# Performance work log

Measured on AMD Instinct MI355X. Metric: run time of the kernel, lower is better.

## Reference

```python
import jax, jax.numpy as jnp
import numpy as np

NUM_ENTITIES = 100000
NUM_TIMES = 10000
D = 512
DB = 768
NUM_REL = 200
NUM_BASES = 4
N_NODES = 30000
N_EDGES = 200000
B = 128
P_ENT = 64
P_TIME = 32
T_UNIQ = 2000


def setup_inputs() -> dict:
    key = jax.random.key(0)
    ks = jax.random.split(key, 32)
    n = jax.random.normal
    ri = jax.random.randint
    inp = {}
    # learned params
    inp['emb'] = n(ks[0], (NUM_ENTITIES + NUM_TIMES, D), jnp.float32) * 0.05
    sc = 1.0 / np.sqrt(D)
    inp['basis1'] = n(ks[1], (NUM_BASES, D, D), jnp.float32) * sc
    inp['att1'] = n(ks[2], (NUM_REL, NUM_BASES), jnp.float32) * 0.5
    inp['root1'] = n(ks[3], (D, D), jnp.float32) * sc
    inp['bias1'] = jnp.zeros((D,), jnp.float32)
    inp['basis2'] = n(ks[4], (NUM_BASES, D, D), jnp.float32) * sc
    inp['att2'] = n(ks[5], (NUM_REL, NUM_BASES), jnp.float32) * 0.5
    inp['root2'] = n(ks[6], (D, D), jnp.float32) * sc
    inp['bias2'] = jnp.zeros((D,), jnp.float32)
    sb = 1.0 / np.sqrt(DB)
    inp['W_lin'] = n(ks[7], (DB, D), jnp.float32) * sb
    inp['b_lin'] = jnp.zeros((D,), jnp.float32)
    inp['W_attn'] = n(ks[8], (DB, D), jnp.float32) * sb
    inp['b_attn'] = jnp.zeros((D,), jnp.float32)
    inp['W_prob'] = n(ks[9], (DB, 1), jnp.float32) * sb
    inp['b_prob'] = jnp.zeros((1,), jnp.float32)
    # forward tensor args
    inp['ques_emb_bert'] = n(ks[10], (B, DB), jnp.float32)
    inp['x_idx'] = ri(ks[11], (N_NODES,), 0, NUM_ENTITIES, jnp.int32)
    inp['edge_index'] = ri(ks[12], (2, N_EDGES), 0, N_NODES, jnp.int32)
    inp['edge_type'] = ri(ks[13], (N_EDGES,), 0, NUM_REL, jnp.int32)
    inp['start_time'] = ri(ks[14], (N_EDGES,), 0, NUM_TIMES, jnp.int32)
    inp['end_time'] = ri(ks[15], (N_EDGES,), 0, NUM_TIMES, jnp.int32)
    inp['edge_batch_idx'] = jnp.sort(ri(ks[16], (N_EDGES,), 0, B, jnp.int32))
    inp['edge_norm'] = jax.random.uniform(ks[17], (N_EDGES,), jnp.float32)
    inp['uniq_times'] = ri(ks[18], (T_UNIQ,), 0, NUM_TIMES, jnp.int32)
    # padded index vectors: positions >= count point at the appended zero row
    ent_counts = ri(ks[19], (B,), 1, P_ENT + 1, jnp.int32)
    time_counts = ri(ks[20], (B,), 1, P_TIME + 1, jnp.int32)
    pe = ri(ks[21], (B, P_ENT), 0, N_NODES, jnp.int32)
    pt = ri(ks[22], (B, P_TIME), 0, T_UNIQ, jnp.int32)
    inp['padded_ent'] = jnp.where(jnp.arange(P_ENT)[None, :] < ent_counts[:, None], pe, N_NODES)
    inp['padded_time'] = jnp.where(jnp.arange(P_TIME)[None, :] < time_counts[:, None], pt, T_UNIQ)
    inp['ent_counts'] = ent_counts
    inp['time_counts'] = time_counts
    return inp


def rgcn_layer(x, basis, att, root, bias, src, dst, etype, st_emb, et_emb, q_t, edge_norm):
    # basis decomposition: project all nodes through each basis once. [N, NB, D]
    xb = jnp.einsum('ni,bio->nbo', x, basis)
    coeff = att[etype]                                 # [E, NB]
    msg = jnp.einsum('eb,ebd->ed', coeff, xb[src])     # [E, D]
    # time gate: question-time embedding vs edge interval midpoint embedding
    gate = jax.nn.sigmoid(jnp.sum(q_t * 0.5 * (st_emb + et_emb), axis=-1))  # [E]
    msg = msg * (gate * edge_norm)[:, None]
    agg = jax.ops.segment_sum(msg, dst, num_segments=N_NODES)
    return agg + x @ root + bias


def reference(emb, basis1, att1, root1, bias1, basis2, att2, root2, bias2,
              W_lin, b_lin, W_attn, b_attn, W_prob, b_prob,
              ques_emb_bert, x_idx, edge_index, edge_type, start_time, end_time,
              edge_batch_idx, edge_norm, uniq_times, padded_ent, padded_time,
              ent_counts, time_counts):
    question_embedding = ques_emb_bert @ W_lin + b_lin                  # [B, D]
    time_for_edge_attn = (ques_emb_bert @ W_attn + b_attn)[edge_batch_idx]  # [E, D]
    st_emb = emb[start_time + NUM_ENTITIES]
    et_emb = emb[end_time + NUM_ENTITIES]
    x = emb[x_idx]                                                      # [N, D]
    src, dst = edge_index[0], edge_index[1]
    h = jax.nn.relu(rgcn_layer(x, basis1, att1, root1, bias1, src, dst, edge_type,
                               st_emb, et_emb, time_for_edge_attn, edge_norm))
    # dropout is identity in eval mode
    h = rgcn_layer(h, basis2, att2, root2, bias2, src, dst, edge_type,
                   st_emb, et_emb, time_for_edge_attn, edge_norm)       # [N, D]
    subgraph_time_emb = emb[uniq_times + NUM_ENTITIES]                  # [T_u, D]
    zero = jnp.zeros((1, D), h.dtype)
    ent_w_zeros = jnp.concatenate([h, zero], axis=0)
    time_w_zeros = jnp.concatenate([subgraph_time_emb, zero], axis=0)
    pooled_ent = jnp.sum(ent_w_zeros[padded_ent], axis=1) / ent_counts[:, None].astype(h.dtype)
    pooled_time = jnp.sum(time_w_zeros[padded_time], axis=1) / time_counts[:, None].astype(h.dtype)
    p_ent = jax.nn.sigmoid(ques_emb_bert @ W_prob + b_prob)             # [B, 1]
    pred = (question_embedding + pooled_ent * p_ent + pooled_time * (1.0 - p_ent)) / 3.0
    # batched cosine similarity against full entity+time vocab
    pred_n = pred / jnp.maximum(jnp.linalg.norm(pred, axis=-1, keepdims=True), 1e-8)
    emb_n = emb / jnp.maximum(jnp.linalg.norm(emb, axis=-1, keepdims=True), 1e-8)
    score = pred_n @ emb_n.T                                            # [B, V]
    return score * 30.0
```

## Files before the change

### kernel.cpp

```cpp
#include <hip/hip_runtime.h>

#define NUM_ENT   100000
#define NTIMES    10000
#define DD        512
#define DB        768
#define NREL      200
#define NBAS      4
#define NN        30000
#define NEDGE     200000
#define BATCH     128
#define PENT      64
#define PTIME     32
#define TUNIQ     2000
#define V_TOT     110000
#define V_PAD     110208
#define VT16      6888
#define M_PAD     30080
#define KT_L      80
#define KT_E      16

typedef __attribute__((ext_vector_type(8))) short s8v;
typedef __attribute__((ext_vector_type(4))) float f4v;

__device__ __forceinline__ unsigned short f2bf(float x){
  unsigned int u = __builtin_bit_cast(unsigned int, x);
  u += 0x7fffu + ((u >> 16) & 1u);
  return (unsigned short)(u >> 16);
}
__device__ __forceinline__ float bf2f(unsigned short h){
  unsigned int u = ((unsigned int)h) << 16;
  return __builtin_bit_cast(float, u);
}

__device__ __forceinline__ void gload16(const void* g, void* l){
  __builtin_amdgcn_global_load_lds(
      (const __attribute__((address_space(1))) void*)g,
      (__attribute__((address_space(3))) void*)l, 16, 0, 0);
}


__global__ __launch_bounds__(256) void k_conv_emb(const float* __restrict__ emb,
    unsigned short* __restrict__ Bp, float* __restrict__ invn){
  int vt = blockIdx.x;
  int wid = threadIdx.x >> 6, lane = threadIdx.x & 63;
  int vrow = vt * 16 + (lane & 15);
  float ss = 0.f;
  __shared__ float ssw[4][16];
  for (int i = 0; i < 4; ++i){
    int kt = wid + i * 4;
    int k0 = kt * 32 + (lane >> 4) * 8;
    s8v o;
    if (vrow < V_TOT){
      const float* p = emb + (size_t)vrow * DD + k0;
      #pragma unroll
      for (int j = 0; j < 8; ++j){ float x = p[j]; ss += x * x; o[j] = (short)f2bf(x); }
    } else {
      #pragma unroll
      for (int j = 0; j < 8; ++j) o[j] = 0;
    }
    *reinterpret_cast<s8v*>(Bp + ((size_t)(kt * VT16 + vt) << 9) + lane * 8) = o;
  }
  ss += __shfl_xor(ss, 16);
  ss += __shfl_xor(ss, 32);
  if ((lane >> 4) == 0) ssw[wid][lane] = ss;
  __syncthreads();
  if (threadIdx.x < 16){
    float s = ssw[0][threadIdx.x] + ssw[1][threadIdx.x] + ssw[2][threadIdx.x] + ssw[3][threadIdx.x];
    int v = vt * 16 + threadIdx.x;
    invn[v] = (v < V_TOT) ? (1.0f / fmaxf(sqrtf(s), 1e-8f)) : 0.0f;
  }
}

__global__ __launch_bounds__(256) void k_small2(const float* __restrict__ ques,
    const float* __restrict__ Wl, const float* __restrict__ bl,
    const float* __restrict__ Wa, const float* __restrict__ ba,
    const float* __restrict__ Wp, const float* __restrict__ bp,
    float* __restrict__ qlin, float* __restrict__ qattn, float* __restrict__ pent){
  if (blockIdx.x == 32){
    int b = threadIdx.x >> 1, half = threadIdx.x & 1;
    float a = 0.f;
    int k0 = half * 384;
    for (int k = k0; k < k0 + 384; ++k)
      a = fmaf(ques[(size_t)b * DB + k], Wp[k], a);
    a += __shfl_xor(a, 1);
    if (half == 0) pent[b] = 1.f / (1.f + expf(-(a + bp[0])));
    return;
  }
  __shared__ float sq[128 * 96];
  int col = threadIdx.x & 31, bg = threadIdx.x >> 5;
  int c0 = blockIdx.x * 32;
  const float* W = (c0 < 512) ? Wl : Wa;
  int wcol = (c0 & 511) + col;
  float acc[16] = {};
  for (int k0 = 0; k0 < DB; k0 += 96){
    __syncthreads();
    for (int i = threadIdx.x; i < 128 * 96; i += 256){
      int b = i / 96, kk = i - b * 96;
      sq[i] = ques[(size_t)b * DB + k0 + kk];
    }
    __syncthreads();
    for (int kk = 0; kk < 96; kk += 4){
      float w0 = W[(size_t)(k0 + kk + 0) * 512 + wcol];
      float w1 = W[(size_t)(k0 + kk + 1) * 512 + wcol];
      float w2 = W[(size_t)(k0 + kk + 2) * 512 + wcol];
      float w3 = W[(size_t)(k0 + kk + 3) * 512 + wcol];
      #pragma unroll
      for (int bb = 0; bb < 16; ++bb){
        float4 qv = *reinterpret_cast<const float4*>(&sq[(bg * 16 + bb) * 96 + kk]);
        acc[bb] = fmaf(qv.x, w0, fmaf(qv.y, w1, fmaf(qv.z, w2, fmaf(qv.w, w3, acc[bb]))));
      }
    }
  }
  float* dst = (c0 < 512) ? qlin : qattn;
  const float* bias = (c0 < 512) ? bl : ba;
  #pragma unroll
  for (int bb = 0; bb < 16; ++bb)
    dst[(size_t)(bg * 16 + bb) * 512 + wcol] = acc[bb] + bias[wcol];
}

__global__ __launch_bounds__(256) void k_pack_qrows(const float* __restrict__ src,
    unsigned short* __restrict__ Ap){
  int w = (int)((blockIdx.x * 256 + threadIdx.x) >> 6);
  int lane = threadIdx.x & 63;
  if (w >= BATCH) return;
  const float* p = src + (size_t)w * 512 + lane * 8;
  s8v o;
  #pragma unroll
  for (int j = 0; j < 8; ++j) o[j] = (short)f2bf(p[j]);
  *reinterpret_cast<s8v*>(Ap + ((size_t)((w >> 4) * KT_E + (lane >> 2)) << 9)
                             + ((w & 15) + (lane & 3) * 16) * 8) = o;
}

__global__ __launch_bounds__(256) void k_pack_B(const float* __restrict__ basis,
    const float* __restrict__ root, unsigned short* __restrict__ Bp){
  int idx = blockIdx.x * 256 + threadIdx.x;
  if (idx >= KT_L * 32 * 64) return;
  int lane = idx & 63; int kt = idx >> 11;
  int k0 = kt * 32 + (lane >> 4) * 8;
  int col = ((idx >> 6) & 31) * 16 + (lane & 15);
  s8v o;
  #pragma unroll
  for (int j = 0; j < 8; ++j){
    int k = k0 + j;
    float v = (k < 2048) ? basis[(size_t)k * 512 + col] : root[(size_t)(k - 2048) * 512 + col];
    o[j] = (short)f2bf(v);
  }
  *reinterpret_cast<s8v*>(Bp + (size_t)idx * 8) = o;
}

template<int MODE, int SWZ>
__global__ __launch_bounds__(256) void k_gemm(
    const unsigned short* __restrict__ A, const unsigned short* __restrict__ B,
    int Kt, int Bt_stride, int ct_off,
    const float* __restrict__ bias, const float* __restrict__ invn,
    float* __restrict__ outf, unsigned short* __restrict__ outh){
  __shared__ __align__(1024) short sAll[3 * 8192];
  int tid = threadIdx.x;
  int lane = tid & 63, wid = tid >> 6;
  int wr = wid >> 1, wc = wid & 1;
  int rt0, ct0;
  if constexpr (SWZ){
    const int q = 117, r = 4;
    int g = blockIdx.x;
    int xcd = g & 7, i = g >> 3;
    int ng = (xcd < r ? xcd * (q + 1) : r * (q + 1) + (xcd - r) * q) + i;
    rt0 = (ng >> 2) * 8;
    ct0 = (ng & 3) * 8;
  } else {
    rt0 = blockIdx.x * 8;
    ct0 = blockIdx.y * 8;
  }
  int ctB = ct0 + ct_off;
  const unsigned short* pA0 = A + ((size_t)(rt0 + 2 * wid) * Kt) * 512 + lane * 8;
  const unsigned short* pA1 = pA0 + (size_t)Kt * 512;
  const unsigned short* pB0 = B + (size_t)(ctB + 2 * wid) * 512 + lane * 8;
  const unsigned short* pB1 = pB0 + 512;
  size_t gbs = (size_t)Bt_stride * 512;
  int so = 2 * wid * 512;
  f4v acc[4][4] = {};

  auto STAGE = [&](int buf, int kt){
    short* b = &sAll[buf * 8192];
    gload16(pA0 + (size_t)kt * 512, b + so);
    gload16(pA1 + (size_t)kt * 512, b + so + 512);
    gload16(pB0 + (size_t)kt * gbs, b + 4096 + so);
    gload16(pB1 + (size_t)kt * gbs, b + 4096 + so + 512);
  };
  auto COMPUTE = [&](int buf){
    const short* base = &sAll[buf * 8192];
    s8v af[4], bfr[4];
    #pragma unroll
    for (int m = 0; m < 4; ++m) af[m] = *reinterpret_cast<const s8v*>(base + (wr * 4 + m) * 512 + lane * 8);
    #pragma unroll
    for (int n = 0; n < 4; ++n) bfr[n] = *reinterpret_cast<const s8v*>(base + 4096 + (wc * 4 + n) * 512 + lane * 8);
    #pragma unroll
    for (int m = 0; m < 4; ++m)
      #pragma unroll
      for (int n = 0; n < 4; ++n)
        acc[m][n] = __builtin_amdgcn_mfma_f32_16x16x32_bf16(af[m], bfr[n], acc[m][n], 0, 0, 0);
  };

  STAGE(0, 0);
  STAGE(1, 1);
  int cb = 0, sb = 2;
  for (int kt = 0; kt < Kt - 2; ++kt){
    STAGE(sb, kt + 2);
    asm volatile("s_waitcnt vmcnt(8)" ::: "memory");
    __builtin_amdgcn_s_barrier();
    __builtin_amdgcn_sched_barrier(0);
    COMPUTE(cb);
    __builtin_amdgcn_s_barrier();
    cb = (cb == 2) ? 0 : cb + 1;
    sb = (sb == 2) ? 0 : sb + 1;
  }
  asm volatile("s_waitcnt vmcnt(4)" ::: "memory");
  __builtin_amdgcn_s_barrier();
  __builtin_amdgcn_sched_barrier(0);
  COMPUTE(cb);
  cb = (cb == 2) ? 0 : cb + 1;
  asm volatile("s_waitcnt vmcnt(0)" ::: "memory");
  __builtin_amdgcn_s_barrier();
  __builtin_amdgcn_sched_barrier(0);
  COMPUTE(cb);

  #pragma unroll
  for (int m = 0; m < 4; ++m)
    #pragma unroll
    for (int n = 0; n < 4; ++n){
      int row0 = rt0 * 16 + (wr * 4 + m) * 16 + ((lane >> 4) * 4);
      int col  = (ct0 + wc * 4 + n) * 16 + (lane & 15);
      #pragma unroll
      for (int r = 0; r < 4; ++r){
        float c = acc[m][n][r];
        int rr = row0 + r;
        if constexpr (MODE == 0){
          if (col < NTIMES) outf[(size_t)rr * NTIMES + col] = c;
        } else if constexpr (MODE == 1){
          if (rr < NN){ float v = fmaxf(c + bias[col], 0.f); outh[(size_t)rr * 512 + col] = f2bf(v); }
        } else if constexpr (MODE == 2){
          if (rr < NN) outf[(size_t)rr * 512 + col] = c + bias[col];
        } else {
          if (col < V_TOT) outf[(size_t)rr * V_TOT + col] = c * invn[col] * 30.0f;
        }
      }
    }
}

__global__ __launch_bounds__(256) void k_edge_w(const int* __restrict__ ebatch,
    const int* __restrict__ st, const int* __restrict__ et,
    const float* __restrict__ enorm, const float* __restrict__ M2,
    float* __restrict__ we){
  int e = blockIdx.x * 256 + threadIdx.x;
  if (e >= NEDGE) return;
  int b = ebatch[e];
  float s = 0.5f * (M2[(size_t)b * NTIMES + st[e]] + M2[(size_t)b * NTIMES + et[e]]);
  we[e] = (1.f / (1.f + expf(-s))) * enorm[e];
}

__global__ __launch_bounds__(256) void k_count(const int* __restrict__ ei,
    int* __restrict__ cnt, int* __restrict__ lists){
  int e = blockIdx.x * 256 + threadIdx.x;
  if (e >= NEDGE) return;
  int dst = ei[NEDGE + e];
  int slot = atomicAdd(&cnt[dst], 1);
  if (slot < 64) lists[(size_t)dst * 64 + slot] = e;
}

__global__ __launch_bounds__(256) void k_gather_x(const int* __restrict__ x_idx,
    const unsigned short* __restrict__ Bp, unsigned short* __restrict__ Ap,
    unsigned short* __restrict__ x_rm){
  int w = (int)((blockIdx.x * 256 + threadIdx.x) >> 6);
  int lane = threadIdx.x & 63;
  if (w >= NN) return;
  int v = x_idx[w];
  s8v x = *reinterpret_cast<const s8v*>(
      Bp + ((size_t)(lane >> 2) * VT16 + (v >> 4)) * 512 + ((v & 15) + (lane & 3) * 16) * 8);
  *reinterpret_cast<s8v*>(x_rm + (size_t)w * 512 + lane * 8) = x;
  *reinterpret_cast<s8v*>(Ap + ((size_t)(w >> 4) * KT_L + 64 + (lane >> 2)) * 512
                             + ((w & 15) + (lane & 3) * 16) * 8) = x;
}

__global__ __launch_bounds__(256) void k_pack_rows(const unsigned short* __restrict__ src_rm,
    unsigned short* __restrict__ Ap){
  int w = (int)((blockIdx.x * 256 + threadIdx.x) >> 6);
  int lane = threadIdx.x & 63;
  if (w >= NN) return;
  s8v x = *reinterpret_cast<const s8v*>(src_rm + (size_t)w * 512 + lane * 8);
  *reinterpret_cast<s8v*>(Ap + ((size_t)(w >> 4) * KT_L + 64 + (lane >> 2)) * 512
                             + ((w & 15) + (lane & 3) * 16) * 8) = x;
}

__global__ __launch_bounds__(256) void k_edge_agg(const unsigned short* __restrict__ xsrc,
    const int* __restrict__ ei, const int* __restrict__ etype,
    const float* __restrict__ we, const float* __restrict__ att,
    const int* __restrict__ cnt, const int* __restrict__ lists,
    unsigned short* __restrict__ Ap){
  __shared__ float satt[NREL * NBAS];
  __shared__ int sed[4][64];
  for (int i = threadIdx.x; i < NREL * NBAS; i += 256) satt[i] = att[i];
  int wid = threadIdx.x >> 6, lane = threadIdx.x & 63;
  int n = blockIdx.x * 4 + wid;
  int deg = min(cnt[n], 64);
  int eid = (lane < deg) ? lists[(size_t)n * 64 + lane] : 0x7fffffff;
  int rank = 0;
  for (int j = 0; j < 64; ++j){
    int v = __shfl(eid, j);
    rank += (v < eid) ? 1 : 0;
  }
  __syncthreads();
  if (lane < deg) sed[wid][rank] = eid;
  __syncthreads();
  float acc[NBAS][8] = {};
  if (deg > 0){
    int my_e = sed[wid][(lane < deg) ? lane : 0];
    int my_s = ei[my_e];
    int my_t = etype[my_e];
    float my_w = we[my_e];
    float c0l = my_w * satt[my_t * 4 + 0];
    float c1l = my_w * satt[my_t * 4 + 1];
    float c2l = my_w * satt[my_t * 4 + 2];
    float c3l = my_w * satt[my_t * 4 + 3];
    int s0 = __shfl(my_s, 0);
    s8v xv = *reinterpret_cast<const s8v*>(xsrc + (size_t)s0 * 512 + lane * 8);
    for (int j = 0; j < deg; ++j){
      s8v xn = xv;
      if (j + 1 < deg){
        int sn = __shfl(my_s, j + 1);
        xn = *reinterpret_cast<const s8v*>(xsrc + (size_t)sn * 512 + lane * 8);
      }
      float c0 = __shfl(c0l, j), c1 = __shfl(c1l, j);
      float c2 = __shfl(c2l, j), c3 = __shfl(c3l, j);
      #pragma unroll
      for (int jj = 0; jj < 8; ++jj){
        float x = bf2f((unsigned short)xv[jj]);
        acc[0][jj] = fmaf(c0, x, acc[0][jj]);
        acc[1][jj] = fmaf(c1, x, acc[1][jj]);
        acc[2][jj] = fmaf(c2, x, acc[2][jj]);
        acc[3][jj] = fmaf(c3, x, acc[3][jj]);
      }
      xv = xn;
    }
  }
  #pragma unroll
  for (int b = 0; b < NBAS; ++b){
    s8v o;
    #pragma unroll
    for (int jj = 0; jj < 8; ++jj) o[jj] = (short)f2bf(acc[b][jj]);
    *reinterpret_cast<s8v*>(Ap + ((size_t)(n >> 4) * KT_L + b * 16 + (lane >> 2)) * 512
                               + ((n & 15) + (lane & 3) * 16) * 8) = o;
  }
}

__global__ __launch_bounds__(256) void k_pred(const float* __restrict__ h2,
    const float* __restrict__ emb, const int* __restrict__ uniq,
    const int* __restrict__ pent_idx, const int* __restrict__ ptime_idx,
    const int* __restrict__ ent_c, const int* __restrict__ time_c,
    const float* __restrict__ qlin, const float* __restrict__ pent,
    unsigned short* __restrict__ Ap_pred){
  int w = (int)((blockIdx.x * 256 + threadIdx.x) >> 6);
  int lane = threadIdx.x & 63;
  if (w >= BATCH) return;
  float ae[8] = {}, at[8] = {};
  for (int j = 0; j < PENT; ++j){
    int idx = pent_idx[w * PENT + j];
    if (idx < NN){
      const float* p = h2 + (size_t)idx * 512 + lane * 8;
      #pragma unroll
      for (int jj = 0; jj < 8; ++jj) ae[jj] += p[jj];
    }
  }
  for (int j = 0; j < PTIME; ++j){
    int ti = ptime_idx[w * PTIME + j];
    if (ti < TUNIQ){
      const float* p = emb + (size_t)(NUM_ENT + uniq[ti]) * 512 + lane * 8;
      #pragma unroll
      for (int jj = 0; jj < 8; ++jj) at[jj] += p[jj];
    }
  }
  float ce = 1.f / (float)ent_c[w], ct = 1.f / (float)time_c[w];
  float p = pent[w];
  float pr[8]; float ss = 0.f;
  #pragma unroll
  for (int jj = 0; jj < 8; ++jj){
    float v = (qlin[(size_t)w * 512 + lane * 8 + jj] + ae[jj] * ce * p + at[jj] * ct * (1.f - p)) * (1.f / 3.f);
    pr[jj] = v; ss += v * v;
  }
  ss += __shfl_xor(ss, 32); ss += __shfl_xor(ss, 16); ss += __shfl_xor(ss, 8);
  ss += __shfl_xor(ss, 4);  ss += __shfl_xor(ss, 2);  ss += __shfl_xor(ss, 1);
  float inv = 1.f / fmaxf(sqrtf(ss), 1e-8f);
  s8v o;
  #pragma unroll
  for (int jj = 0; jj < 8; ++jj) o[jj] = (short)f2bf(pr[jj] * inv);
  *reinterpret_cast<s8v*>(Ap_pred + ((size_t)((w >> 4) * KT_E + (lane >> 2)) << 9)
                                  + ((w & 15) + (lane & 3) * 16) * 8) = o;
}

extern "C" void kernel_launch(void* const* d_in, const int* in_sizes, int n_in,
                              void* d_out, int out_size, void* d_ws, size_t ws_size,
                              hipStream_t stream){
  const float* emb    = (const float*)d_in[0];
  const float* basis1 = (const float*)d_in[1];
  const float* att1   = (const float*)d_in[2];
  const float* root1  = (const float*)d_in[3];
  const float* bias1  = (const float*)d_in[4];
  const float* basis2 = (const float*)d_in[5];
  const float* att2   = (const float*)d_in[6];
  const float* root2  = (const float*)d_in[7];
  const float* bias2  = (const float*)d_in[8];
  const float* W_lin  = (const float*)d_in[9];
  const float* b_lin  = (const float*)d_in[10];
  const float* W_attn = (const float*)d_in[11];
  const float* b_attn = (const float*)d_in[12];
  const float* W_prob = (const float*)d_in[13];
  const float* b_prob = (const float*)d_in[14];
  const float* ques   = (const float*)d_in[15];
  const int* x_idx    = (const int*)d_in[16];
  const int* eidx     = (const int*)d_in[17];
  const int* etype    = (const int*)d_in[18];
  const int* stime    = (const int*)d_in[19];
  const int* etime    = (const int*)d_in[20];
  const int* ebatch   = (const int*)d_in[21];
  const float* enorm  = (const float*)d_in[22];
  const int* uniq     = (const int*)d_in[23];
  const int* pent_i   = (const int*)d_in[24];
  const int* ptime_i  = (const int*)d_in[25];
  const int* ent_c    = (const int*)d_in[26];
  const int* time_c   = (const int*)d_in[27];
  float* out = (float*)d_out;

  char* w = (char*)d_ws;
  size_t off = 0;
  auto alloc = [&](size_t bytes)->char*{ char* p = w + off; off += (bytes + 255) & ~(size_t)255; return p; };
  unsigned short* Bp_emb = (unsigned short*)alloc((size_t)KT_E * VT16 * 1024);
  float*          invn   = (float*)alloc((size_t)V_PAD * 4);
  unsigned short* Ap     = (unsigned short*)alloc((size_t)(M_PAD / 16) * KT_L * 1024);
  unsigned short* B1p    = (unsigned short*)alloc((size_t)KT_L * 32 * 1024);
  unsigned short* B2p    = (unsigned short*)alloc((size_t)KT_L * 32 * 1024);
  char* xh_base = alloc((size_t)NN * 512 * 2 * 2);
  unsigned short* x_rm = (unsigned short*)xh_base;
  unsigned short* h1   = (unsigned short*)(xh_base + (size_t)NN * 512 * 2);
  float*          h2   = (float*)xh_base;
  float* M2    = (float*)alloc((size_t)BATCH * NTIMES * 4);
  float* we    = (float*)alloc((size_t)NEDGE * 4);
  float* qlin  = (float*)alloc((size_t)BATCH * 512 * 4);
  float* qattn = (float*)alloc((size_t)BATCH * 512 * 4);
  float* pent  = (float*)alloc(1024);
  unsigned short* Apq    = (unsigned short*)alloc((size_t)8 * KT_E * 1024);
  unsigned short* Appred = (unsigned short*)alloc((size_t)8 * KT_E * 1024);
  int* cnt   = (int*)alloc((size_t)NN * 4);
  int* lists = (int*)alloc((size_t)NN * 64 * 4);
  (void)ws_size; (void)in_sizes; (void)n_in; (void)out_size;

  k_conv_emb<<<VT16, 256, 0, stream>>>(emb, Bp_emb, invn);
  k_small2<<<33, 256, 0, stream>>>(ques, W_lin, b_lin, W_attn, b_attn, W_prob, b_prob,
                                   qlin, qattn, pent);
  k_pack_qrows<<<32, 256, 0, stream>>>(qattn, Apq);
  k_pack_B<<<(KT_L * 32 * 64 + 255) / 256, 256, 0, stream>>>(basis1, root1, B1p);
  k_pack_B<<<(KT_L * 32 * 64 + 255) / 256, 256, 0, stream>>>(basis2, root2, B2p);
  k_gemm<0,0><<<dim3(1, 79), 256, 0, stream>>>(Apq, Bp_emb, KT_E, VT16, NUM_ENT / 16,
                                               nullptr, nullptr, M2, nullptr);
  k_edge_w<<<(NEDGE + 255) / 256, 256, 0, stream>>>(ebatch, stime, etime, enorm, M2, we);
  hipMemsetAsync(cnt, 0, (size_t)NN * 4, stream);
  k_count<<<(NEDGE + 255) / 256, 256, 0, stream>>>(eidx, cnt, lists);
  k_gather_x<<<NN / 4, 256, 0, stream>>>(x_idx, Bp_emb, Ap, x_rm);
  k_edge_agg<<<NN / 4, 256, 0, stream>>>(x_rm, eidx, etype, we, att1, cnt, lists, Ap);
  k_gemm<1,1><<<940, 256, 0, stream>>>(Ap, B1p, KT_L, 32, 0,
                                       bias1, nullptr, nullptr, h1);
  k_pack_rows<<<NN / 4, 256, 0, stream>>>(h1, Ap);
  k_edge_agg<<<NN / 4, 256, 0, stream>>>(h1, eidx, etype, we, att2, cnt, lists, Ap);
  k_gemm<2,1><<<940, 256, 0, stream>>>(Ap, B2p, KT_L, 32, 0,
                                       bias2, nullptr, h2, nullptr);
  k_pred<<<32, 256, 0, stream>>>(h2, emb, uniq, pent_i, ptime_i, ent_c, time_c,
                                 qlin, pent, Appred);
  k_gemm<3,0><<<dim3(1, V_PAD / 128), 256, 0, stream>>>(Appred, Bp_emb, KT_E, VT16, 0,
                                                        nullptr, invn, out, nullptr);
}
```

Measured before the change: 789.0 us.

## Use 256x256-tile 512-thread GEMM for RGCN layers and store layer-2 output as bf16

The two RGCN layer GEMMs move from 128x128 tiles with 256 threads to 256x256 tiles with 512 threads (8 waves, 8x4 MFMA accumulators each). The grid is XCD-swizzled over 236 blocks, and s_setprio is raised around the MFMA loop. The aim is more data reuse per LDS load and less global traffic. The layer-2 output is now written as bf16 instead of fp32, which halves that write and the later reads in k_pred at some precision cost. Embedding conversion also switches to float4 loads. The A buffer grows to cover the padded rows of the larger tiles. The larger tiles bring more register pressure and only 236 blocks, which may underfill the CUs.

```diff
diff --git a/kernel.cpp b/kernel.cpp
--- a/kernel.cpp
+++ b/kernel.cpp
@@ -15,7 +15,8 @@
 #define V_TOT     110000
 #define V_PAD     110208
 #define VT16      6888
-#define M_PAD     30080
+#define M_PAD2    30208
+#define MT2R      1888
 #define KT_L      80
 #define KT_E      16
 
@@ -51,9 +52,14 @@
     int k0 = kt * 32 + (lane >> 4) * 8;
     s8v o;
     if (vrow < V_TOT){
-      const float* p = emb + (size_t)vrow * DD + k0;
-      #pragma unroll
-      for (int j = 0; j < 8; ++j){ float x = p[j]; ss += x * x; o[j] = (short)f2bf(x); }
+      const float4* p = reinterpret_cast<const float4*>(emb + (size_t)vrow * DD + k0);
+      float4 v0 = p[0], v1 = p[1];
+      ss += v0.x*v0.x + v0.y*v0.y + v0.z*v0.z + v0.w*v0.w;
+      ss += v1.x*v1.x + v1.y*v1.y + v1.z*v1.z + v1.w*v1.w;
+      o[0] = (short)f2bf(v0.x); o[1] = (short)f2bf(v0.y);
+      o[2] = (short)f2bf(v0.z); o[3] = (short)f2bf(v0.w);
+      o[4] = (short)f2bf(v1.x); o[5] = (short)f2bf(v1.y);
+      o[6] = (short)f2bf(v1.z); o[7] = (short)f2bf(v1.w);
     } else {
       #pragma unroll
       for (int j = 0; j < 8; ++j) o[j] = 0;
@@ -148,56 +154,51 @@
   *reinterpret_cast<s8v*>(Bp + (size_t)idx * 8) = o;
 }
 
-template<int MODE, int SWZ>
-__global__ __launch_bounds__(256) void k_gemm(
+template<int MODE>
+__global__ __launch_bounds__(512, 2) void k_gemm256(
     const unsigned short* __restrict__ A, const unsigned short* __restrict__ B,
-    int Kt, int Bt_stride, int ct_off,
-    const float* __restrict__ bias, const float* __restrict__ invn,
-    float* __restrict__ outf, unsigned short* __restrict__ outh){
-  __shared__ __align__(1024) short sAll[3 * 8192];
+    const float* __restrict__ bias, unsigned short* __restrict__ outh){
+  __shared__ __align__(1024) short sAll[3 * 16384];
+  const int Kt = KT_L;
   int tid = threadIdx.x;
   int lane = tid & 63, wid = tid >> 6;
-  int wr = wid >> 1, wc = wid & 1;
-  int rt0, ct0;
-  if constexpr (SWZ){
-    const int q = 117, r = 4;
-    int g = blockIdx.x;
-    int xcd = g & 7, i = g >> 3;
-    int ng = (xcd < r ? xcd * (q + 1) : r * (q + 1) + (xcd - r) * q) + i;
-    rt0 = (ng >> 2) * 8;
-    ct0 = (ng & 3) * 8;
-  } else {
-    rt0 = blockIdx.x * 8;
-    ct0 = blockIdx.y * 8;
-  }
-  int ctB = ct0 + ct_off;
-  const unsigned short* pA0 = A + ((size_t)(rt0 + 2 * wid) * Kt) * 512 + lane * 8;
-  const unsigned short* pA1 = pA0 + (size_t)Kt * 512;
-  const unsigned short* pB0 = B + (size_t)(ctB + 2 * wid) * 512 + lane * 8;
-  const unsigned short* pB1 = pB0 + 512;
-  size_t gbs = (size_t)Bt_stride * 512;
-  int so = 2 * wid * 512;
-  f4v acc[4][4] = {};
+  int wr = wid >> 2, wc = wid & 3;
+  const int q = 29, r = 4;
+  int g = blockIdx.x;
+  int xcd = g & 7, i = g >> 3;
+  int ng = (xcd < r ? xcd * (q + 1) : r * (q + 1) + (xcd - r) * q) + i;
+  int blkM = ng >> 1, blkN = ng & 1;
+  int rt0 = blkM * 16;
+  int ct0 = blkN * 16;
+  const unsigned short* pA0 = A + ((size_t)(rt0 + wid) * Kt) * 512 + lane * 8;
+  const unsigned short* pA1 = A + ((size_t)(rt0 + 8 + wid) * Kt) * 512 + lane * 8;
+  const unsigned short* pB0 = B + (size_t)(ct0 + wid) * 512 + lane * 8;
+  const unsigned short* pB1 = B + (size_t)(ct0 + 8 + wid) * 512 + lane * 8;
+  const size_t gbs = 32 * 512;
+  int soA0 = wid * 512, soA1 = (8 + wid) * 512;
+  f4v acc[8][4] = {};
 
   auto STAGE = [&](int buf, int kt){
-    short* b = &sAll[buf * 8192];
-    gload16(pA0 + (size_t)kt * 512, b + so);
-    gload16(pA1 + (size_t)kt * 512, b + so + 512);
-    gload16(pB0 + (size_t)kt * gbs, b + 4096 + so);
-    gload16(pB1 + (size_t)kt * gbs, b + 4096 + so + 512);
+    short* b = &sAll[buf * 16384];
+    gload16(pA0 + (size_t)kt * 512, b + soA0);
+    gload16(pA1 + (size_t)kt * 512, b + soA1);
+    gload16(pB0 + (size_t)kt * gbs, b + 8192 + soA0);
+    gload16(pB1 + (size_t)kt * gbs, b + 8192 + soA1);
   };
   auto COMPUTE = [&](int buf){
-    const short* base = &sAll[buf * 8192];
-    s8v af[4], bfr[4];
-    #pragma unroll
-    for (int m = 0; m < 4; ++m) af[m] = *reinterpret_cast<const s8v*>(base + (wr * 4 + m) * 512 + lane * 8);
-    #pragma unroll
-    for (int n = 0; n < 4; ++n) bfr[n] = *reinterpret_cast<const s8v*>(base + 4096 + (wc * 4 + n) * 512 + lane * 8);
-    #pragma unroll
-    for (int m = 0; m < 4; ++m)
+    const short* base = &sAll[buf * 16384];
+    s8v af[8], bfr[4];
+    #pragma unroll
+    for (int m = 0; m < 8; ++m) af[m] = *reinterpret_cast<const s8v*>(base + (wr * 8 + m) * 512 + lane * 8);
+    #pragma unroll
+    for (int n = 0; n < 4; ++n) bfr[n] = *reinterpret_cast<const s8v*>(base + 8192 + (wc * 4 + n) * 512 + lane * 8);
+    __builtin_amdgcn_s_setprio(1);
+    #pragma unroll
+    for (int m = 0; m < 8; ++m)
       #pragma unroll
       for (int n = 0; n < 4; ++n)
         acc[m][n] = __builtin_amdgcn_mfma_f32_16x16x32_bf16(af[m], bfr[n], acc[m][n], 0, 0, 0);
+    __builtin_amdgcn_s_setprio(0);
   };
 
   STAGE(0, 0);
@@ -223,6 +224,90 @@
   __builtin_amdgcn_sched_barrier(0);
   COMPUTE(cb);
 
+  int R0 = blkM * 256 + wr * 128 + (lane >> 4) * 4;
+  int C0 = blkN * 256 + wc * 64 + (lane & 15);
+  #pragma unroll
+  for (int m = 0; m < 8; ++m)
+    #pragma unroll
+    for (int n = 0; n < 4; ++n){
+      int col = C0 + n * 16;
+      float bb = bias[col];
+      #pragma unroll
+      for (int rr4 = 0; rr4 < 4; ++rr4){
+        int rr = R0 + m * 16 + rr4;
+        if (rr < NN){
+          float v = acc[m][n][rr4] + bb;
+          if constexpr (MODE == 1) v = fmaxf(v, 0.f);
+          outh[(size_t)rr * 512 + col] = f2bf(v);
+        }
+      }
+    }
+}
+
+template<int MODE>
+__global__ __launch_bounds__(256) void k_gemm(
+    const unsigned short* __restrict__ A, const unsigned short* __restrict__ B,
+    int Kt, int Bt_stride, int ct_off,
+    const float* __restrict__ invn, float* __restrict__ outf){
+  __shared__ __align__(1024) short sAll[3 * 8192];
+  int tid = threadIdx.x;
+  int lane = tid & 63, wid = tid >> 6;
+  int wr = wid >> 1, wc = wid & 1;
+  int rt0 = blockIdx.x * 8;
+  int ct0 = blockIdx.y * 8;
+  int ctB = ct0 + ct_off;
+  const unsigned short* pA0 = A + ((size_t)(rt0 + 2 * wid) * Kt) * 512 + lane * 8;
+  const unsigned short* pA1 = pA0 + (size_t)Kt * 512;
+  const unsigned short* pB0 = B + (size_t)(ctB + 2 * wid) * 512 + lane * 8;
+  const unsigned short* pB1 = pB0 + 512;
+  size_t gbs = (size_t)Bt_stride * 512;
+  int so = 2 * wid * 512;
+  f4v acc[4][4] = {};
+
+  auto STAGE = [&](int buf, int kt){
+    short* b = &sAll[buf * 8192];
+    gload16(pA0 + (size_t)kt * 512, b + so);
+    gload16(pA1 + (size_t)kt * 512, b + so + 512);
+    gload16(pB0 + (size_t)kt * gbs, b + 4096 + so);
+    gload16(pB1 + (size_t)kt * gbs, b + 4096 + so + 512);
+  };
+  auto COMPUTE = [&](int buf){
+    const short* base = &sAll[buf * 8192];
+    s8v af[4], bfr[4];
+    #pragma unroll
+    for (int m = 0; m < 4; ++m) af[m] = *reinterpret_cast<const s8v*>(base + (wr * 4 + m) * 512 + lane * 8);
+    #pragma unroll
+    for (int n = 0; n < 4; ++n) bfr[n] = *reinterpret_cast<const s8v*>(base + 4096 + (wc * 4 + n) * 512 + lane * 8);
+    #pragma unroll
+    for (int m = 0; m < 4; ++m)
+      #pragma unroll
+      for (int n = 0; n < 4; ++n)
+        acc[m][n] = __builtin_amdgcn_mfma_f32_16x16x32_bf16(af[m], bfr[n], acc[m][n], 0, 0, 0);
+  };
+
+  STAGE(0, 0);
+  STAGE(1, 1);
+  int cb = 0, sb = 2;
+  for (int kt = 0; kt < Kt - 2; ++kt){
+    STAGE(sb, kt + 2);
+    asm volatile("s_waitcnt vmcnt(8)" ::: "memory");
+    __builtin_amdgcn_s_barrier();
+    __builtin_amdgcn_sched_barrier(0);
+    COMPUTE(cb);
+    __builtin_amdgcn_s_barrier();
+    cb = (cb == 2) ? 0 : cb + 1;
+    sb = (sb == 2) ? 0 : sb + 1;
+  }
+  asm volatile("s_waitcnt vmcnt(4)" ::: "memory");
+  __builtin_amdgcn_s_barrier();
+  __builtin_amdgcn_sched_barrier(0);
+  COMPUTE(cb);
+  cb = (cb == 2) ? 0 : cb + 1;
+  asm volatile("s_waitcnt vmcnt(0)" ::: "memory");
+  __builtin_amdgcn_s_barrier();
+  __builtin_amdgcn_sched_barrier(0);
+  COMPUTE(cb);
+
   #pragma unroll
   for (int m = 0; m < 4; ++m)
     #pragma unroll
@@ -235,10 +320,6 @@
         int rr = row0 + r;
         if constexpr (MODE == 0){
           if (col < NTIMES) outf[(size_t)rr * NTIMES + col] = c;
-        } else if constexpr (MODE == 1){
-          if (rr < NN){ float v = fmaxf(c + bias[col], 0.f); outh[(size_t)rr * 512 + col] = f2bf(v); }
-        } else if constexpr (MODE == 2){
-          if (rr < NN) outf[(size_t)rr * 512 + col] = c + bias[col];
         } else {
           if (col < V_TOT) outf[(size_t)rr * V_TOT + col] = c * invn[col] * 30.0f;
         }
@@ -351,7 +432,7 @@
   }
 }
 
-__global__ __launch_bounds__(256) void k_pred(const float* __restrict__ h2,
+__global__ __launch_bounds__(256) void k_pred(const unsigned short* __restrict__ h2,
     const float* __restrict__ emb, const int* __restrict__ uniq,
     const int* __restrict__ pent_idx, const int* __restrict__ ptime_idx,
     const int* __restrict__ ent_c, const int* __restrict__ time_c,
@@ -364,9 +445,9 @@
   for (int j = 0; j < PENT; ++j){
     int idx = pent_idx[w * PENT + j];
     if (idx < NN){
-      const float* p = h2 + (size_t)idx * 512 + lane * 8;
-      #pragma unroll
-      for (int jj = 0; jj < 8; ++jj) ae[jj] += p[jj];
+      s8v hv = *reinterpret_cast<const s8v*>(h2 + (size_t)idx * 512 + lane * 8);
+      #pragma unroll
+      for (int jj = 0; jj < 8; ++jj) ae[jj] += bf2f((unsigned short)hv[jj]);
     }
   }
   for (int j = 0; j < PTIME; ++j){
@@ -433,13 +514,13 @@
   auto alloc = [&](size_t bytes)->char*{ char* p = w + off; off += (bytes + 255) & ~(size_t)255; return p; };
   unsigned short* Bp_emb = (unsigned short*)alloc((size_t)KT_E * VT16 * 1024);
   float*          invn   = (float*)alloc((size_t)V_PAD * 4);
-  unsigned short* Ap     = (unsigned short*)alloc((size_t)(M_PAD / 16) * KT_L * 1024);
+  unsigned short* Ap     = (unsigned short*)alloc((size_t)MT2R * KT_L * 1024);
   unsigned short* B1p    = (unsigned short*)alloc((size_t)KT_L * 32 * 1024);
   unsigned short* B2p    = (unsigned short*)alloc((size_t)KT_L * 32 * 1024);
   char* xh_base = alloc((size_t)NN * 512 * 2 * 2);
   unsigned short* x_rm = (unsigned short*)xh_base;
   unsigned short* h1   = (unsigned short*)(xh_base + (size_t)NN * 512 * 2);
-  float*          h2   = (float*)xh_base;
+  unsigned short* h2   = (unsigned short*)xh_base;
   float* M2    = (float*)alloc((size_t)BATCH * NTIMES * 4);
   float* we    = (float*)alloc((size_t)NEDGE * 4);
   float* qlin  = (float*)alloc((size_t)BATCH * 512 * 4);
@@ -457,21 +538,19 @@
   k_pack_qrows<<<32, 256, 0, stream>>>(qattn, Apq);
   k_pack_B<<<(KT_L * 32 * 64 + 255) / 256, 256, 0, stream>>>(basis1, root1, B1p);
   k_pack_B<<<(KT_L * 32 * 64 + 255) / 256, 256, 0, stream>>>(basis2, root2, B2p);
-  k_gemm<0,0><<<dim3(1, 79), 256, 0, stream>>>(Apq, Bp_emb, KT_E, VT16, NUM_ENT / 16,
-                                               nullptr, nullptr, M2, nullptr);
+  k_gemm<0><<<dim3(1, 79), 256, 0, stream>>>(Apq, Bp_emb, KT_E, VT16, NUM_ENT / 16,
+                                             nullptr, M2);
   k_edge_w<<<(NEDGE + 255) / 256, 256, 0, stream>>>(ebatch, stime, etime, enorm, M2, we);
   hipMemsetAsync(cnt, 0, (size_t)NN * 4, stream);
   k_count<<<(NEDGE + 255) / 256, 256, 0, stream>>>(eidx, cnt, lists);
   k_gather_x<<<NN / 4, 256, 0, stream>>>(x_idx, Bp_emb, Ap, x_rm);
   k_edge_agg<<<NN / 4, 256, 0, stream>>>(x_rm, eidx, etype, we, att1, cnt, lists, Ap);
-  k_gemm<1,1><<<940, 256, 0, stream>>>(Ap, B1p, KT_L, 32, 0,
-                                       bias1, nullptr, nullptr, h1);
+  k_gemm256<1><<<236, 512, 0, stream>>>(Ap, B1p, bias1, h1);
   k_pack_rows<<<NN / 4, 256, 0, stream>>>(h1, Ap);
   k_edge_agg<<<NN / 4, 256, 0, stream>>>(h1, eidx, etype, we, att2, cnt, lists, Ap);
-  k_gemm<2,1><<<940, 256, 0, stream>>>(Ap, B2p, KT_L, 32, 0,
-                                       bias2, nullptr, h2, nullptr);
+  k_gemm256<2><<<236, 512, 0, stream>>>(Ap, B2p, bias2, h2);
   k_pred<<<32, 256, 0, stream>>>(h2, emb, uniq, pent_i, ptime_i, ent_c, time_c,
                                  qlin, pent, Appred);
-  k_gemm<3,0><<<dim3(1, V_PAD / 128), 256, 0, stream>>>(Appred, Bp_emb, KT_E, VT16, 0,
-                                                        nullptr, invn, out, nullptr);
-}
+  k_gemm<3><<<dim3(1, V_PAD / 128), 256, 0, stream>>>(Appred, Bp_emb, KT_E, VT16, 0,
+                                                      invn, out);
+}
```

Result: faster. 764.6 us (-3.1%).
